# Performance work log

Measured on AMD Instinct MI355X. Metric: run time of the kernel, lower is better.

The kernel has to match this reference:

```python
import jax, jax.numpy as jnp
import numpy as np

DIM = 2048
HEAD_DIM = 128
H = DIM // HEAD_DIM          # num ttt heads = 16
D_H = 128                    # inter_multi = 1.0 -> d_h = head_dim
CHUNK = 2048                 # lact_chunk_size
B, L = 1, 8192
BASE_LR = 0.01
LN_EPS = 1e-6                # flax LayerNorm default
NS_COEFS = [(4.0848, -6.8946, 2.927), (3.9505, -6.3029, 2.6377),
            (3.7418, -5.5913, 2.3037), (2.8769, -3.1427, 1.2046),
            (2.8366, -3.0525, 1.2012)]


def silu(x):
    return x * jax.nn.sigmoid(x)


def silu_backprop(dy, x):
    s = jax.nn.sigmoid(x)
    return dy * s * (1 + x * (1 - s))


def l2_norm(x, eps=1e-5):
    return x / (jnp.linalg.norm(x, axis=-1, keepdims=True) + eps)


def zeropower_ns5(G):
    # 5-step Newton-Schulz orthogonalization on a batch of matrices (bh, m, n)
    X = G
    transposed = G.shape[1] > G.shape[2]
    if transposed:
        X = jnp.swapaxes(X, 1, 2)
    X = X / (jnp.linalg.norm(X, axis=(1, 2), keepdims=True) + 1e-7)
    for a, b, c in NS_COEFS:
        A = X @ jnp.swapaxes(X, 1, 2)
        Bm = b * A + c * (A @ A)
        X = a * X + Bm @ X
    if transposed:
        X = jnp.swapaxes(X, 1, 2)
    return X


def block_causal_lact_swiglu(w0, w1, w2, q, k, v, lr0, lr1, lr2, momentum):
    # w0,w2: (bh, d_h, d); w1: (bh, d, d_h); q,k,v: (bh, l, d); lr*: (bh, l, 1)
    bh, l, d = k.shape
    v = jnp.swapaxes(v, 1, 2)   # (bh, d, l)
    q = jnp.swapaxes(q, 1, 2)   # (bh, d, l)
    w0_norm = jnp.linalg.norm(w0, axis=2, keepdims=True)
    w1_norm = jnp.linalg.norm(w1, axis=2, keepdims=True)
    w2_norm = jnp.linalg.norm(w2, axis=2, keepdims=True)
    outs = []
    for i in range(0, l - CHUNK, CHUNK):
        s, e = i, i + CHUNK
        ki = k[:, s:e, :]                      # (bh, C, d)
        vi = v[:, :, s:e]                      # (bh, d, C)
        qi = q[:, :, s:e]                      # (bh, d, C)
        lr0i, lr1i, lr2i = lr0[:, s:e, :], lr1[:, s:e, :], lr2[:, s:e, :]
        # apply current fast weights to queries
        h = w2 @ qi                            # (bh, d_h, C)
        gate = silu(w0 @ qi)
        outs.append(w1 @ (gate * h))           # (bh, d, C)
        # manual SwiGLU backprop through keys to get fast-weight grads
        kiT = jnp.swapaxes(ki, 1, 2)           # (bh, d, C)
        gate_before = w0 @ kiT                 # (bh, d_h, C)
        hidden_before = w2 @ kiT               # (bh, d_h, C)
        hidden = silu(gate_before) * hidden_before
        dhidden = jnp.swapaxes(w1, 1, 2) @ vi  # (bh, d_h, C)
        dhidden_before = dhidden * silu(gate_before)
        dgate = dhidden * hidden_before
        dgate_before = silu_backprop(dgate, gate_before)
        lr1iT = jnp.swapaxes(lr1i, 1, 2)       # (bh, 1, C) per-token lr
        dw1 = vi @ jnp.swapaxes(hidden * lr1iT, 1, 2)   # (bh, d, d_h)
        dw0 = dgate_before @ (ki * lr0i)                # (bh, d_h, d)
        dw2 = dhidden_before @ (ki * lr2i)              # (bh, d_h, d)
        if momentum is not None:
            m_i = jnp.mean(momentum[:, s:e, :], axis=1, keepdims=True)  # (bh,1,1)
            dw0 = dw0 + dw0 * m_i
            dw1 = dw1 + dw1 * m_i
            dw2 = dw2 + dw2 * m_i
        dw0 = zeropower_ns5(dw0)
        dw1 = zeropower_ns5(dw1)
        dw2 = zeropower_ns5(dw2)
        w0 = w0 + dw0
        w1 = w1 + dw1
        w2 = w2 + dw2
        # renormalize rows back to the initial norms
        w0 = w0 / (jnp.linalg.norm(w0, axis=2, keepdims=True) + 1e-5) * w0_norm
        w1 = w1 / (jnp.linalg.norm(w1, axis=2, keepdims=True) + 1e-5) * w1_norm
        w2 = w2 / (jnp.linalg.norm(w2, axis=2, keepdims=True) + 1e-5) * w2_norm
    # final chunk: apply only
    qi = q[:, :, l - CHUNK:]
    h = w2 @ qi
    gate = silu(w0 @ qi)
    outs.append(w1 @ (gate * h))
    out = jnp.concatenate(outs, axis=2)        # (bh, d, l)
    return jnp.swapaxes(out, 1, 2)             # (bh, l, d)


def _forward(x, W_qkv, W_lr, W_o, W_m, b_m, W_s, b_s, ln_g, ln_b, w0, w1, w2):
    b, l, _ = x.shape
    h, d = H, HEAD_DIM
    qkv = silu(x @ W_qkv).reshape(b, l, h, 3 * d)
    ttt_q, ttt_k, ttt_v = jnp.split(qkv, 3, axis=-1)
    ttt_q = l2_norm(ttt_q).reshape(b * h, l, d)
    ttt_k = l2_norm(ttt_k).reshape(b * h, l, d)
    ttt_v = ttt_v.reshape(b * h, l, d)
    base_lr_inv = BASE_LR + jnp.log(-jnp.expm1(jnp.float32(-BASE_LR)))
    lr = jax.nn.softplus(x @ W_lr + base_lr_inv)                 # (b, l, 3h)
    lr = lr.reshape(b, l, 3, h).transpose(2, 0, 3, 1).reshape(3, b * h, l, 1)
    lr0, lr1, lr2 = lr[0], lr[1], lr[2]
    w0b = jnp.tile(w0, (b, 1, 1))
    w1b = jnp.tile(w1, (b, 1, 1))
    w2b = jnp.tile(w2, (b, 1, 1))
    momentum = jax.nn.sigmoid(x @ W_m + b_m)                     # (b, l, h)
    momentum = momentum.reshape(b, l, h, 1).transpose(0, 2, 1, 3).reshape(b * h, l, 1)
    out = block_causal_lact_swiglu(w0b, w1b, w2b, ttt_q, ttt_k, ttt_v,
                                   lr0, lr1, lr2, momentum)      # (bh, l, d)
    # LayerNorm over last dim (flax default eps)
    mu = jnp.mean(out, axis=-1, keepdims=True)
    var = jnp.mean(jnp.square(out - mu), axis=-1, keepdims=True)
    out = (out - mu) * jax.lax.rsqrt(var + LN_EPS) * ln_g + ln_b
    scale = silu(x @ W_s + b_s).reshape(b, l, h, 1).transpose(0, 2, 1, 3).reshape(b * h, l, 1)
    out = out * scale
    out = out.reshape(b, h, l, d).transpose(0, 2, 1, 3).reshape(b, l, h * d)
    return out @ W_o


def setup_inputs() -> dict:
    ks = jax.random.split(jax.random.key(0), 11)
    sd = 1.0 / np.sqrt(DIM)
    return {
        "x": jax.random.normal(ks[0], (B, L, DIM), jnp.float32),
        "W_qkv": jax.random.normal(ks[1], (DIM, 3 * DIM), jnp.float32) * sd,
        "W_lr": jax.random.normal(ks[2], (DIM, 3 * H), jnp.float32) * sd,
        "W_o": jax.random.normal(ks[3], (DIM, DIM), jnp.float32) * sd,
        "W_m": jax.random.normal(ks[4], (DIM, H), jnp.float32) * sd,
        "b_m": jnp.zeros((H,), jnp.float32),
        "W_s": jax.random.normal(ks[5], (DIM, H), jnp.float32) * sd,
        "b_s": jnp.zeros((H,), jnp.float32),
        "ln_g": jnp.ones((HEAD_DIM,), jnp.float32),
        "ln_b": jnp.zeros((HEAD_DIM,), jnp.float32),
        "w0": jax.random.normal(ks[6], (H, D_H, HEAD_DIM), jnp.float32) / np.sqrt(HEAD_DIM),
        "w1": jax.random.normal(ks[7], (H, HEAD_DIM, D_H), jnp.float32) / np.sqrt(D_H),
        "w2": jax.random.normal(ks[8], (H, D_H, HEAD_DIM), jnp.float32) / np.sqrt(HEAD_DIM),
    }


def reference(x, W_qkv, W_lr, W_o, W_m, b_m, W_s, b_s, ln_g, ln_b, w0, w1, w2):
    return _forward(x, W_qkv, W_lr, W_o, W_m, b_m, W_s, b_s, ln_g, ln_b, w0, w1, w2)
```

## Files before the change

### kernel.cpp

```cpp
#include <hip/hip_runtime.h>
#include <hip/hip_bf16.h>
#include <cstdint>
#include <cstddef>

#define LSEQ   8192
#define DMODEL 2048
#define NH     16
#define HD     128
#define CH     2048

typedef __attribute__((ext_vector_type(8))) __bf16 bf16x8;
typedef __attribute__((ext_vector_type(4))) float f32x4;


__device__ __forceinline__ float wave_sum64(float v) {
#pragma unroll
  for (int m = 32; m; m >>= 1) v += __shfl_xor(v, m, 64);
  return v;
}

__device__ __forceinline__ float sigm(float x) { return 1.0f / (1.0f + expf(-x)); }

__device__ __forceinline__ unsigned short f2bf(float f) {
  unsigned int u = __float_as_uint(f);
  u += 0x7FFFu + ((u >> 16) & 1u);
  return (unsigned short)(u >> 16);
}
__device__ __forceinline__ float bf2f(unsigned short h) {
  return __uint_as_float((unsigned int)h << 16);
}

__device__ __forceinline__ void gload_lds16(const void* g, void* l) {
  __builtin_amdgcn_global_load_lds((__attribute__((address_space(1))) void*)(g),
                                   (__attribute__((address_space(3))) void*)(l), 16, 0, 0);
}

union bfu8 { bf16x8 v; unsigned short u[8]; };


__global__ void k_cast(const float* __restrict__ X, unsigned short* __restrict__ Xb, int n4) {
  int i = blockIdx.x * 256 + threadIdx.x;
  int stride = gridDim.x * 256;
  for (; i < n4; i += stride) {
    float4 v = ((const float4*)X)[i];
    ushort4 o;
    o.x = f2bf(v.x); o.y = f2bf(v.y); o.z = f2bf(v.z); o.w = f2bf(v.w);
    ((ushort4*)Xb)[i] = o;
  }
}

__global__ void k_tcast(const float* __restrict__ W, unsigned short* __restrict__ Wt,
                        int K, int N) {
  __shared__ float t[64][65];
  const int n0 = blockIdx.x * 64, k0 = blockIdx.y * 64;
  const int tid = threadIdx.x;
  const int cx = tid & 63, ry = tid >> 6;
#pragma unroll
  for (int r = 0; r < 16; ++r) {
    int row = ry + r * 4;
    t[row][cx] = W[(size_t)(k0 + row) * N + n0 + cx];
  }
  __syncthreads();
#pragma unroll
  for (int r = 0; r < 16; ++r) {
    int nn = ry + r * 4;
    Wt[(size_t)(n0 + nn) * K + k0 + cx] = f2bf(t[cx][nn]);
  }
}


__device__ __forceinline__ void gemm_core(const unsigned short* __restrict__ A,
                                          const unsigned short* __restrict__ B,
                                          int K, int ldA, int ldB, int row0, int col0,
                                          unsigned short* Al, unsigned short* Bl,
                                          f32x4 acc[4][4]) {
  const int tid = threadIdx.x;
  const int w = tid >> 6, l = tid & 63;
  const int lrow = l & 15, lk = (l >> 4) * 8;
  const int wr = (w >> 1) * 64, wc = (w & 1) * 64;
  const int srow = l >> 2, skk = (l & 3) * 8;

  for (int kk = 0; kk < K; kk += 32) {
#pragma unroll
    for (int q = 0; q < 2; ++q) {
      int c = w * 2 + q;
      gload_lds16(A + (size_t)(row0 + c * 16 + srow) * ldA + kk + skk, &Al[c * 512]);
      gload_lds16(B + (size_t)(col0 + c * 16 + srow) * ldB + kk + skk, &Bl[c * 512]);
    }
    __syncthreads();
    bf16x8 af[4], bfr[4];
#pragma unroll
    for (int m = 0; m < 4; ++m)
      af[m] = *(const bf16x8*)&Al[(wr + m * 16 + lrow) * 32 + lk];
#pragma unroll
    for (int n = 0; n < 4; ++n)
      bfr[n] = *(const bf16x8*)&Bl[(wc + n * 16 + lrow) * 32 + lk];
#pragma unroll
    for (int m = 0; m < 4; ++m)
#pragma unroll
      for (int n = 0; n < 4; ++n)
        acc[m][n] = __builtin_amdgcn_mfma_f32_16x16x32_bf16(af[m], bfr[n], acc[m][n], 0, 0, 0);
    __syncthreads();
  }
}


__device__ __forceinline__ bf16x8 ld_sw(const unsigned short* base, int row, int kcol) {
  int byte = (row * 256 + kcol * 2) ^ ((row & 7) << 4);
  return *(const bf16x8*)((const char*)base + byte);
}
__device__ __forceinline__ void st_sw(unsigned short* base, int row, int col, unsigned short v) {
  int byte = (row * 256 + col * 2) ^ ((row & 7) << 4);
  *(unsigned short*)((char*)base + byte) = v;
}
__device__ __forceinline__ unsigned short ld_sw1(const unsigned short* base, int row, int col) {
  int byte = (row * 256 + col * 2) ^ ((row & 7) << 4);
  return *(const unsigned short*)((const char*)base + byte);
}

__device__ __forceinline__ void stage_sw(const float* __restrict__ src, int ld,
                                         unsigned short* dst, int tid) {
#pragma unroll
  for (int p = 0; p < 16; ++p) {
    int row = p * 8 + (tid >> 5);
    int col = (tid & 31) * 4;
    float4 v = *(const float4*)(src + (size_t)row * ld + col);
    int byte = (row * 256 + col * 2) ^ ((row & 7) << 4);
    unsigned short* d = (unsigned short*)((char*)dst + byte);
    d[0] = f2bf(v.x); d[1] = f2bf(v.y); d[2] = f2bf(v.z); d[3] = f2bf(v.w);
  }
}

__device__ __forceinline__ void stage_sw64(const float* __restrict__ src, int ld,
                                           unsigned short* dst, int tid) {
#pragma unroll
  for (int p = 0; p < 8; ++p) {
    int row = p * 8 + (tid >> 5);
    int col = (tid & 31) * 4;
    float4 v = *(const float4*)(src + (size_t)row * ld + col);
    int byte = (row * 256 + col * 2) ^ ((row & 7) << 4);
    unsigned short* d = (unsigned short*)((char*)dst + byte);
    d[0] = f2bf(v.x); d[1] = f2bf(v.y); d[2] = f2bf(v.z); d[3] = f2bf(v.w);
  }
}

__device__ __forceinline__ void stage_hl(const float* __restrict__ src, int ld,
                                         unsigned short* H, unsigned short* L, int tid) {
#pragma unroll
  for (int p = 0; p < 16; ++p) {
    int row = p * 8 + (tid >> 5);
    int col = (tid & 31) * 4;
    float4 v = *(const float4*)(src + (size_t)row * ld + col);
    int byte = (row * 256 + col * 2) ^ ((row & 7) << 4);
    unsigned short* h = (unsigned short*)((char*)H + byte);
    unsigned short* l = (unsigned short*)((char*)L + byte);
    const float* pv = (const float*)&v;
#pragma unroll
    for (int i = 0; i < 4; ++i) {
      unsigned short hi = f2bf(pv[i]);
      h[i] = hi;
      l[i] = f2bf(pv[i] - bf2f(hi));
    }
  }
}

__device__ __forceinline__ void stage_hl_1024(const float* __restrict__ src, int ld,
                                              unsigned short* H, unsigned short* L, int tid) {
#pragma unroll
  for (int p = 0; p < 4; ++p) {
    int row = p * 32 + (tid >> 5);
    int col = (tid & 31) * 4;
    float4 v = *(const float4*)(src + (size_t)row * ld + col);
    int byte = (row * 256 + col * 2) ^ ((row & 7) << 4);
    unsigned short* h = (unsigned short*)((char*)H + byte);
    unsigned short* l = (unsigned short*)((char*)L + byte);
    const float* pv = (const float*)&v;
#pragma unroll
    for (int i = 0; i < 4; ++i) {
      unsigned short hi = f2bf(pv[i]);
      h[i] = hi;
      l[i] = f2bf(pv[i] - bf2f(hi));
    }
  }
}

__device__ __forceinline__ void stage_hl_ts(const float* __restrict__ src, int ld,
                                            const float* __restrict__ lr,
                                            unsigned short* H, unsigned short* L, int tid) {
#pragma unroll
  for (int p = 0; p < 16; ++p) {
    int t = p * 8 + (tid >> 5);
    int d = (tid & 31) * 4;
    float4 v = *(const float4*)(src + (size_t)t * ld + d);
    float sc = lr[t];
    const float* pv = (const float*)&v;
#pragma unroll
    for (int i = 0; i < 4; ++i) {
      float x = pv[i] * sc;
      unsigned short hi = f2bf(x);
      st_sw(H, d + i, t, hi);
      st_sw(L, d + i, t, f2bf(x - bf2f(hi)));
    }
  }
}


__global__ void k_init_w(const float* __restrict__ w0, const float* __restrict__ w1,
                         const float* __restrict__ w2, float* __restrict__ WW,
                         float* __restrict__ WN0, float* __restrict__ W1T) {
  int rid = blockIdx.x;
  int m = rid >> 11;
  int gr = rid & 2047;
  const float* src = (m == 0) ? w0 : (m == 1) ? w1 : w2;
  const float* row = src + (size_t)gr * HD;
  float* drow = WW + ((size_t)m * 2048 + gr) * HD;
  int l = threadIdx.x;
  float v0 = row[l], v1 = row[l + 64];
  drow[l] = v0; drow[l + 64] = v1;
  if (m == 1) {
    int g = gr >> 7, r = gr & 127;
    W1T[((size_t)g * 128 + l) * 128 + r] = v0;
    W1T[((size_t)g * 128 + l + 64) * 128 + r] = v1;
  }
  float s = wave_sum64(v0 * v0 + v1 * v1);
  if (l == 0) WN0[rid] = sqrtf(s);
}


__global__ __launch_bounds__(256) void k_qkv_mfma(const unsigned short* __restrict__ xb,
                                                  const unsigned short* __restrict__ Wqt,
                                                  float* __restrict__ Q, float* __restrict__ Km,
                                                  float* __restrict__ V) {
  __shared__ unsigned short Al[128 * 32];
  __shared__ unsigned short Bl[128 * 32];
  __shared__ float nrm[128][2];
  const int bx = blockIdx.x, ct = blockIdx.y;

  f32x4 acc[4][4];
#pragma unroll
  for (int m = 0; m < 4; ++m)
#pragma unroll
    for (int n = 0; n < 4; ++n) acc[m][n] = {};

  gemm_core(xb, Wqt, DMODEL, DMODEL, DMODEL, bx * 128, ct * 128, Al, Bl, acc);

  const int hh = ct / 3, which = ct % 3;
  float* dst = (which == 0) ? Q : (which == 1) ? Km : V;
  const int tid = threadIdx.x, w = tid >> 6, l = tid & 63;
  const int wr = (w >> 1) * 64, wc = (w & 1) * 64;

#pragma unroll
  for (int m = 0; m < 4; ++m)
#pragma unroll
    for (int n = 0; n < 4; ++n)
#pragma unroll
      for (int j = 0; j < 4; ++j) {
        float v = acc[m][n][j];
        acc[m][n][j] = v * sigm(v);
      }

  float f[4][4];
  if (which != 2) {
#pragma unroll
    for (int m = 0; m < 4; ++m)
#pragma unroll
      for (int j = 0; j < 4; ++j) {
        float p = 0.0f;
#pragma unroll
        for (int n = 0; n < 4; ++n) p = fmaf(acc[m][n][j], acc[m][n][j], p);
        p += __shfl_xor(p, 1, 64);
        p += __shfl_xor(p, 2, 64);
        p += __shfl_xor(p, 4, 64);
        p += __shfl_xor(p, 8, 64);
        f[m][j] = p;
      }
    if ((l & 15) == 0) {
#pragma unroll
      for (int m = 0; m < 4; ++m)
#pragma unroll
        for (int j = 0; j < 4; ++j)
          nrm[wr + m * 16 + (l >> 4) * 4 + j][w & 1] = f[m][j];
    }
    __syncthreads();
#pragma unroll
    for (int m = 0; m < 4; ++m)
#pragma unroll
      for (int j = 0; j < 4; ++j) {
        int row = wr + m * 16 + (l >> 4) * 4 + j;
        f[m][j] = 1.0f / (sqrtf(nrm[row][0] + nrm[row][1]) + 1e-5f);
      }
  } else {
#pragma unroll
    for (int m = 0; m < 4; ++m)
#pragma unroll
      for (int j = 0; j < 4; ++j) f[m][j] = 1.0f;
  }

#pragma unroll
  for (int m = 0; m < 4; ++m)
#pragma unroll
    for (int j = 0; j < 4; ++j) {
      int t = bx * 128 + wr + m * 16 + (l >> 4) * 4 + j;
      int fth = t * NH + hh;
      int g = fth >> 13, tp = fth & 8191;
      float* drow = dst + ((size_t)g * LSEQ + tp) * HD;
#pragma unroll
      for (int n = 0; n < 4; ++n)
        drow[wc + n * 16 + (l & 15)] = acc[m][n][j] * f[m][j];
    }
}


__global__ __launch_bounds__(256) void k_lrms5(const float* __restrict__ x,
                                               const float* __restrict__ Wlr,
                                               const float* __restrict__ Wsc,
                                               float* __restrict__ P) {
  __shared__ float Xs[128][67];
  __shared__ float Ws[128][68];
  const int tb = blockIdx.x;
  const int kp = blockIdx.y;
  const int tid = threadIdx.x;
  for (int i = tid; i < 128 * 64; i += 256) {
    int k = i >> 6, c = i & 63;
    float wv = (c < 48) ? Wlr[(size_t)(kp * 128 + k) * 48 + c]
                        : Wsc[(size_t)(kp * 128 + k) * 16 + (c - 48)];
    Ws[k][c] = wv;
  }
  const int t8 = tid >> 5, kk = tid & 31;
#pragma unroll
  for (int r = 0; r < 8; ++r) {
    int t = t8 + r * 8;
    float4 v = *(const float4*)(x + (size_t)(tb * 64 + t) * DMODEL + kp * 128 + kk * 4);
    Xs[kk * 4 + 0][t] = v.x; Xs[kk * 4 + 1][t] = v.y;
    Xs[kk * 4 + 2][t] = v.z; Xs[kk * 4 + 3][t] = v.w;
  }
  __syncthreads();
  const int ty = tid >> 4, tx = tid & 15;
  float acc[4][4];
#pragma unroll
  for (int i = 0; i < 4; ++i)
#pragma unroll
    for (int j = 0; j < 4; ++j) acc[i][j] = 0.0f;
  for (int k = 0; k < 128; ++k) {
    float a[4], b[4];
#pragma unroll
    for (int i = 0; i < 4; ++i) a[i] = Xs[k][ty * 4 + i];
#pragma unroll
    for (int j = 0; j < 4; ++j) b[j] = Ws[k][tx * 4 + j];
#pragma unroll
    for (int i = 0; i < 4; ++i)
#pragma unroll
      for (int j = 0; j < 4; ++j) acc[i][j] = fmaf(a[i], b[j], acc[i][j]);
  }
  float* o = P + ((size_t)tb * 16 + kp) * 4096;
#pragma unroll
  for (int i = 0; i < 4; ++i)
#pragma unroll
    for (int j = 0; j < 4; ++j)
      o[(ty * 4 + i) * 64 + tx * 4 + j] = acc[i][j];
}

__global__ void k_lrsum(const float* __restrict__ P, const float* __restrict__ bs,
                        float* __restrict__ LR, float* __restrict__ SCL) {
  int e = blockIdx.x * 256 + threadIdx.x;
  int t = e >> 6, c = e & 63;
  const float* base = P + ((size_t)(t >> 6) * 16) * 4096 + (t & 63) * 64 + c;
  float sum = 0.0f;
#pragma unroll
  for (int kp = 0; kp < 16; ++kp) sum += base[(size_t)kp * 4096];
  if (c < 48) {
    float base_lr_inv = 0.01f + logf(-expm1f(-0.01f));
    float v = sum + base_lr_inv;
    float sp = fmaxf(v, 0.0f) + log1pf(expf(-fabsf(v)));
    LR[(size_t)c * LSEQ + t] = sp;
  } else {
    float v = sum + bs[c - 48];
    SCL[(size_t)(c - 48) * LSEQ + t] = v * sigm(v);
  }
}


__global__ __launch_bounds__(256) void k_out2(const float* __restrict__ WW,
                                              const float* __restrict__ Q,
                                              const float* __restrict__ SCL,
                                              const float* __restrict__ lng,
                                              const float* __restrict__ lnb,
                                              unsigned short* __restrict__ U, int s) {
  __shared__ __align__(16) char smem[81920];
  unsigned short* Qs  = (unsigned short*)smem;
  unsigned short* W0s = (unsigned short*)(smem + 16384);
  unsigned short* W2s = (unsigned short*)(smem + 49152);
  float* Os = (float*)(smem + 16384);

  const int g = blockIdx.y;
  const int t0 = blockIdx.x * 64;
  const int tid = threadIdx.x;
  const int w = tid >> 6, l = tid & 63;
  const int lrow = l & 15, lk8 = (l >> 4) * 8;
  const int wr = (w >> 1) * 32, wc = (w & 1) * 64;

  const float* Qg  = Q + ((size_t)g * LSEQ + s + t0) * HD;
  const float* w0g = WW + ((size_t)0 * 2048 + g * 128) * 128;
  const float* w1g = WW + ((size_t)1 * 2048 + g * 128) * 128;
  const float* w2g = WW + ((size_t)2 * 2048 + g * 128) * 128;

  stage_sw64(Qg, HD, Qs, tid);
  stage_sw(w0g, 128, W0s, tid);
  stage_sw(w2g, 128, W2s, tid);
  __syncthreads();

  f32x4 ga[2][4], ha[2][4];
#pragma unroll
  for (int m = 0; m < 2; ++m)
#pragma unroll
    for (int n = 0; n < 4; ++n) { ga[m][n] = {}; ha[m][n] = {}; }
#pragma unroll
  for (int kk = 0; kk < 128; kk += 32) {
    bf16x8 af[2], b0[4], b2[4];
#pragma unroll
    for (int m = 0; m < 2; ++m) af[m] = ld_sw(Qs, wr + m * 16 + lrow, kk + lk8);
#pragma unroll
    for (int n = 0; n < 4; ++n) {
      b0[n] = ld_sw(W0s, wc + n * 16 + lrow, kk + lk8);
      b2[n] = ld_sw(W2s, wc + n * 16 + lrow, kk + lk8);
    }
#pragma unroll
    for (int m = 0; m < 2; ++m)
#pragma unroll
      for (int n = 0; n < 4; ++n) {
        ga[m][n] = __builtin_amdgcn_mfma_f32_16x16x32_bf16(af[m], b0[n], ga[m][n], 0, 0, 0);
        ha[m][n] = __builtin_amdgcn_mfma_f32_16x16x32_bf16(af[m], b2[n], ha[m][n], 0, 0, 0);
      }
  }
  __syncthreads();
#pragma unroll
  for (int m = 0; m < 2; ++m)
#pragma unroll
    for (int n = 0; n < 4; ++n)
#pragma unroll
      for (int j = 0; j < 4; ++j) {
        int row = wr + m * 16 + (l >> 4) * 4 + j;
        int col = wc + n * 16 + (l & 15);
        float gv = ga[m][n][j];
        st_sw(Qs, row, col, f2bf(gv * sigm(gv) * ha[m][n][j]));
      }
  stage_sw(w1g, 128, W0s, tid);
  __syncthreads();

  f32x4 oa[2][4];
#pragma unroll
  for (int m = 0; m < 2; ++m)
#pragma unroll
    for (int n = 0; n < 4; ++n) oa[m][n] = {};
#pragma unroll
  for (int kk = 0; kk < 128; kk += 32) {
    bf16x8 af[2], b1[4];
#pragma unroll
    for (int m = 0; m < 2; ++m) af[m] = ld_sw(Qs, wr + m * 16 + lrow, kk + lk8);
#pragma unroll
    for (int n = 0; n < 4; ++n) b1[n] = ld_sw(W0s, wc + n * 16 + lrow, kk + lk8);
#pragma unroll
    for (int m = 0; m < 2; ++m)
#pragma unroll
      for (int n = 0; n < 4; ++n)
        oa[m][n] = __builtin_amdgcn_mfma_f32_16x16x32_bf16(af[m], b1[n], oa[m][n], 0, 0, 0);
  }
  __syncthreads();
#pragma unroll
  for (int m = 0; m < 2; ++m)
#pragma unroll
    for (int n = 0; n < 4; ++n)
#pragma unroll
      for (int j = 0; j < 4; ++j) {
        int row = wr + m * 16 + (l >> 4) * 4 + j;
        int col = wc + n * 16 + (l & 15);
        Os[row * 132 + col] = oa[m][n][j];
      }
  __syncthreads();

  const int tok = tid >> 2, part = tid & 3;
  const float* orow = Os + tok * 132 + part * 32;
  float sum = 0.0f;
#pragma unroll
  for (int q = 0; q < 8; ++q) {
    float4 v = *(const float4*)(orow + q * 4);
    sum += (v.x + v.y) + (v.z + v.w);
  }
  sum += __shfl_xor(sum, 1, 64);
  sum += __shfl_xor(sum, 2, 64);
  float mu = sum * (1.0f / 128.0f);
  float vs = 0.0f;
#pragma unroll
  for (int q = 0; q < 8; ++q) {
    float4 v = *(const float4*)(orow + q * 4);
    float d0 = v.x - mu, d1 = v.y - mu, d2 = v.z - mu, d3 = v.w - mu;
    vs += d0 * d0 + d1 * d1 + d2 * d2 + d3 * d3;
  }
  vs += __shfl_xor(vs, 1, 64);
  vs += __shfl_xor(vs, 2, 64);
  float rstd = rsqrtf(vs * (1.0f / 128.0f) + 1e-6f);
  int tabs = s + t0 + tok;
  float sc = SCL[(size_t)g * LSEQ + tabs];
  unsigned short* urow = U + (size_t)tabs * DMODEL + g * HD + part * 32;
#pragma unroll
  for (int q = 0; q < 8; ++q) {
    float4 v = *(const float4*)(orow + q * 4);
    int d = part * 32 + q * 4;
    ushort4 o;
    o.x = f2bf(((v.x - mu) * rstd * lng[d + 0] + lnb[d + 0]) * sc);
    o.y = f2bf(((v.y - mu) * rstd * lng[d + 1] + lnb[d + 1]) * sc);
    o.z = f2bf(((v.z - mu) * rstd * lng[d + 2] + lnb[d + 2]) * sc);
    o.w = f2bf(((v.w - mu) * rstd * lng[d + 3] + lnb[d + 3]) * sc);
    *(ushort4*)(urow + q * 4) = o;
  }
}


__global__ __launch_bounds__(1024) void k_fe(const float* __restrict__ WW,
                                             const float* __restrict__ W1T,
                                             const float* __restrict__ Km,
                                             const float* __restrict__ V,
                                             float* __restrict__ BUF, int s) {
  __shared__ __align__(16) char smem[131072];
  unsigned short* KH = (unsigned short*)smem;
  unsigned short* KL = (unsigned short*)(smem + 32768);
  unsigned short* VH = (unsigned short*)(smem + 65536);
  unsigned short* VL = (unsigned short*)(smem + 98304);

  const int tt0 = blockIdx.x * 128;
  const int g = blockIdx.y;
  const int tid = threadIdx.x;
  const int w = tid >> 6, l = tid & 63;
  const int ww = w >> 2, wv = w & 3;
  const int lrow = l & 15, lk8 = (l >> 4) * 8;
  const int frow = (l >> 4) * 4, fcol = l & 15;

  stage_hl_1024(Km + ((size_t)g * LSEQ + s + tt0) * HD, HD, KH, KL, tid);
  stage_hl_1024(V + ((size_t)g * LSEQ + s + tt0) * HD, HD, VH, VL, tid);
  __syncthreads();

  const float* Asrc[3];
  Asrc[0] = WW + ((size_t)0 * 2048 + g * 128) * 128;
  Asrc[1] = WW + ((size_t)2 * 2048 + g * 128) * 128;
  Asrc[2] = W1T + (size_t)g * 16384;

  f32x4 acc[3][2][2];
#pragma unroll
  for (int q = 0; q < 3; ++q)
#pragma unroll
    for (int m = 0; m < 2; ++m)
#pragma unroll
      for (int n = 0; n < 2; ++n) acc[q][m][n] = {};

#pragma unroll 1
  for (int q = 0; q < 3; ++q) {
    const float* src = Asrc[q];
    const unsigned short* BH = (q == 2) ? VH : KH;
    const unsigned short* BL = (q == 2) ? VL : KL;
#pragma unroll
    for (int kk = 0; kk < 128; kk += 32) {
      bf16x8 ah[2], al[2], bh[2], bl[2];
#pragma unroll
      for (int m = 0; m < 2; ++m) {
        int row = ww * 32 + m * 16 + lrow;
        float4 v0 = *(const float4*)(src + (size_t)row * 128 + kk + lk8);
        float4 v1 = *(const float4*)(src + (size_t)row * 128 + kk + lk8 + 4);
        bfu8 h, lo;
        const float* p0 = (const float*)&v0;
        const float* p1 = (const float*)&v1;
#pragma unroll
        for (int i = 0; i < 4; ++i) {
          unsigned short hb0 = f2bf(p0[i]);
          h.u[i] = hb0; lo.u[i] = f2bf(p0[i] - bf2f(hb0));
          unsigned short hb1 = f2bf(p1[i]);
          h.u[i + 4] = hb1; lo.u[i + 4] = f2bf(p1[i] - bf2f(hb1));
        }
        ah[m] = h.v; al[m] = lo.v;
      }
#pragma unroll
      for (int n = 0; n < 2; ++n) {
        int row = wv * 32 + n * 16 + lrow;
        bh[n] = ld_sw(BH, row, kk + lk8);
        bl[n] = ld_sw(BL, row, kk + lk8);
      }
#pragma unroll
      for (int m = 0; m < 2; ++m)
#pragma unroll
        for (int n = 0; n < 2; ++n) {
          acc[q][m][n] = __builtin_amdgcn_mfma_f32_16x16x32_bf16(ah[m], bh[n], acc[q][m][n], 0, 0, 0);
          acc[q][m][n] = __builtin_amdgcn_mfma_f32_16x16x32_bf16(ah[m], bl[n], acc[q][m][n], 0, 0, 0);
          acc[q][m][n] = __builtin_amdgcn_mfma_f32_16x16x32_bf16(al[m], bh[n], acc[q][m][n], 0, 0, 0);
        }
    }
  }

  float* out0 = BUF + (size_t)0 * (NH * 128 * CH) + (size_t)g * 128 * CH;
  float* out1 = BUF + (size_t)1 * (NH * 128 * CH) + (size_t)g * 128 * CH;
  float* out2 = BUF + (size_t)2 * (NH * 128 * CH) + (size_t)g * 128 * CH;
#pragma unroll
  for (int m = 0; m < 2; ++m)
#pragma unroll
    for (int n = 0; n < 2; ++n)
#pragma unroll
      for (int j = 0; j < 4; ++j) {
        int row = ww * 32 + m * 16 + frow + j;
        int col = wv * 32 + n * 16 + fcol;
        float gb = acc[0][m][n][j];
        float hb = acc[1][m][n][j];
        float dh = acc[2][m][n][j];
        float sg = sigm(gb);
        float sgb = gb * sg;
        float hid = sgb * hb;
        float dgate = dh * hb;
        float dgb = dgate * sg * (1.0f + gb * (1.0f - sg));
        float dhb = dh * sgb;
        size_t o = (size_t)row * CH + tt0 + col;
        out0[o] = hid; out1[o] = dgb; out2[o] = dhb;
      }
}

__global__ __launch_bounds__(256) void k_dwp_mx(const float* __restrict__ BUF,
                                                const float* __restrict__ Km,
                                                const float* __restrict__ V,
                                                const float* __restrict__ LR,
                                                float* __restrict__ DWP, int s) {
  __shared__ __align__(16) char smem[131072];
  unsigned short* AH = (unsigned short*)smem;
  unsigned short* AL = (unsigned short*)(smem + 32768);
  unsigned short* BH = (unsigned short*)(smem + 65536);
  unsigned short* BL = (unsigned short*)(smem + 98304);

  const int p = blockIdx.x;
  const int g = blockIdx.y;
  const int z = blockIdx.z;
  const int tid = threadIdx.x;
  const int w = tid >> 6, l = tid & 63;
  const int lrow = l & 15, lk8 = (l >> 4) * 8;
  const int wr = (w >> 1) * 64, wc = (w & 1) * 64;

  const int msel = (z == 0) ? 1 : (z == 1) ? 0 : 2;
  const float* M = BUF + (size_t)msel * (NH * 128 * CH) + (size_t)g * 128 * CH;
  const float* N = (z == 1) ? V : Km;
  const float* lr = LR + (size_t)(z * NH + g) * LSEQ;
  const int ts = p * 256;

  f32x4 acc[4][4];
#pragma unroll
  for (int m = 0; m < 4; ++m)
#pragma unroll
    for (int n = 0; n < 4; ++n) acc[m][n] = {};

  for (int h = 0; h < 2; ++h) {
    if (h) __syncthreads();
    stage_hl(M + ts + h * 128, CH, AH, AL, tid);
    stage_hl_ts(N + ((size_t)g * LSEQ + s + ts + h * 128) * HD, HD,
                lr + s + ts + h * 128, BH, BL, tid);
    __syncthreads();
#pragma unroll
    for (int kk = 0; kk < 128; kk += 32) {
      bf16x8 ah[4], al4[4], bh[4], bl4[4];
#pragma unroll
      for (int m = 0; m < 4; ++m) {
        ah[m] = ld_sw(AH, wr + m * 16 + lrow, kk + lk8);
        al4[m] = ld_sw(AL, wr + m * 16 + lrow, kk + lk8);
      }
#pragma unroll
      for (int n = 0; n < 4; ++n) {
        bh[n] = ld_sw(BH, wc + n * 16 + lrow, kk + lk8);
        bl4[n] = ld_sw(BL, wc + n * 16 + lrow, kk + lk8);
      }
#pragma unroll
      for (int m = 0; m < 4; ++m)
#pragma unroll
        for (int n = 0; n < 4; ++n) {
          acc[m][n] = __builtin_amdgcn_mfma_f32_16x16x32_bf16(ah[m], bh[n], acc[m][n], 0, 0, 0);
          acc[m][n] = __builtin_amdgcn_mfma_f32_16x16x32_bf16(ah[m], bl4[n], acc[m][n], 0, 0, 0);
          acc[m][n] = __builtin_amdgcn_mfma_f32_16x16x32_bf16(al4[m], bh[n], acc[m][n], 0, 0, 0);
        }
    }
  }

  float* outp = DWP + (((size_t)(z * NH + g)) * 8 + p) * 16384;
#pragma unroll
  for (int m = 0; m < 4; ++m)
#pragma unroll
    for (int n = 0; n < 4; ++n)
#pragma unroll
      for (int j = 0; j < 4; ++j) {
        int row = wr + m * 16 + (l >> 4) * 4 + j;
        int col = wc + n * 16 + (l & 15);
        outp[row * 128 + col] = acc[m][n][j];
      }
}

__global__ __launch_bounds__(1024) void k_ns5_mfma(const float* __restrict__ DWP,
                                                   float* __restrict__ DW) {
  __shared__ __align__(16) char smem[131072];
  unsigned short* PH = (unsigned short*)smem;
  unsigned short* PL = (unsigned short*)(smem + 32768);
  unsigned short* QH = (unsigned short*)(smem + 65536);
  unsigned short* QL = (unsigned short*)(smem + 98304);
  float* red = (float*)(smem + 65536);

  const float NA[5] = {4.0848f, 3.9505f, 3.7418f, 2.8769f, 2.8366f};
  const float NB[5] = {-6.8946f, -6.3029f, -5.5913f, -3.1427f, -3.0525f};
  const float NC[5] = {2.927f, 2.6377f, 2.3037f, 1.2046f, 1.2012f};
  const int zg = blockIdx.x;
  const int z = zg >> 4;
  const float* base = DWP + (size_t)zg * 8 * 16384;
  float* Gout = DW + (size_t)zg * 16384;
  const int tid = threadIdx.x;
  const int w = tid >> 6, l = tid & 63;
  const int ww = w >> 2, wv = w & 3;
  const int lrow = l & 15, lk8 = (l >> 4) * 8;
  const int frow = (l >> 4) * 4, fcol = l & 15;

  float vals[16];
  float psum = 0.0f;
#pragma unroll
  for (int r = 0; r < 16; ++r) {
    int idx = tid + r * 1024;
    float sv = 0.0f;
#pragma unroll
    for (int p = 0; p < 8; ++p) sv += base[(size_t)p * 16384 + idx];
    vals[r] = sv;
    psum = fmaf(sv, sv, psum);
  }
  psum = wave_sum64(psum);
  if (l == 0) red[w] = psum;
  __syncthreads();
  float tot = 0.0f;
#pragma unroll
  for (int i = 0; i < 16; ++i) tot += red[i];
  float scl = 1.0f / (sqrtf(tot) + 1e-7f);
  __syncthreads();
#pragma unroll
  for (int r = 0; r < 16; ++r) {
    int idx = tid + r * 1024;
    int rr = idx >> 7, cc = idx & 127;
    float v = vals[r] * scl;
    unsigned short hi = f2bf(v);
    st_sw(PH, rr, cc, hi);
    st_sw(PL, rr, cc, f2bf(v - bf2f(hi)));
  }
  __syncthreads();

#pragma unroll 1
  for (int it = 0; it < 5; ++it) {
    const float ac = NA[it], bc = NB[it], cc2 = NC[it];

    f32x4 accA[2][2];
#pragma unroll
    for (int m = 0; m < 2; ++m)
#pragma unroll
      for (int n = 0; n < 2; ++n) accA[m][n] = {};
#pragma unroll
    for (int kk = 0; kk < 128; kk += 32) {
      bf16x8 ah[2], al[2], bh[2], bl[2];
#pragma unroll
      for (int m = 0; m < 2; ++m) {
        ah[m] = ld_sw(PH, ww * 32 + m * 16 + lrow, kk + lk8);
        al[m] = ld_sw(PL, ww * 32 + m * 16 + lrow, kk + lk8);
      }
#pragma unroll
      for (int n = 0; n < 2; ++n) {
        bh[n] = ld_sw(PH, wv * 32 + n * 16 + lrow, kk + lk8);
        bl[n] = ld_sw(PL, wv * 32 + n * 16 + lrow, kk + lk8);
      }
#pragma unroll
      for (int m = 0; m < 2; ++m)
#pragma unroll
        for (int n = 0; n < 2; ++n) {
          accA[m][n] = __builtin_amdgcn_mfma_f32_16x16x32_bf16(ah[m], bh[n], accA[m][n], 0, 0, 0);
          accA[m][n] = __builtin_amdgcn_mfma_f32_16x16x32_bf16(ah[m], bl[n], accA[m][n], 0, 0, 0);
          accA[m][n] = __builtin_amdgcn_mfma_f32_16x16x32_bf16(al[m], bh[n], accA[m][n], 0, 0, 0);
        }
    }
#pragma unroll
    for (int m = 0; m < 2; ++m)
#pragma unroll
      for (int n = 0; n < 2; ++n)
#pragma unroll
        for (int j = 0; j < 4; ++j) {
          int row = ww * 32 + m * 16 + frow + j;
          int col = wv * 32 + n * 16 + fcol;
          float v = accA[m][n][j];
          unsigned short hi = f2bf(v);
          st_sw(QH, row, col, hi);
          st_sw(QL, row, col, f2bf(v - bf2f(hi)));
        }
    __syncthreads();

    f32x4 accB[2][2];
#pragma unroll
    for (int m = 0; m < 2; ++m)
#pragma unroll
      for (int n = 0; n < 2; ++n) accB[m][n] = {};
#pragma unroll
    for (int kk = 0; kk < 128; kk += 32) {
      bf16x8 ah[2], al[2], bh[2], bl[2];
#pragma unroll
      for (int m = 0; m < 2; ++m) {
        ah[m] = ld_sw(QH, ww * 32 + m * 16 + lrow, kk + lk8);
        al[m] = ld_sw(QL, ww * 32 + m * 16 + lrow, kk + lk8);
      }
#pragma unroll
      for (int n = 0; n < 2; ++n) {
        bh[n] = ld_sw(QH, wv * 32 + n * 16 + lrow, kk + lk8);
        bl[n] = ld_sw(QL, wv * 32 + n * 16 + lrow, kk + lk8);
      }
#pragma unroll
      for (int m = 0; m < 2; ++m)
#pragma unroll
        for (int n = 0; n < 2; ++n) {
          accB[m][n] = __builtin_amdgcn_mfma_f32_16x16x32_bf16(ah[m], bh[n], accB[m][n], 0, 0, 0);
          accB[m][n] = __builtin_amdgcn_mfma_f32_16x16x32_bf16(ah[m], bl[n], accB[m][n], 0, 0, 0);
          accB[m][n] = __builtin_amdgcn_mfma_f32_16x16x32_bf16(al[m], bh[n], accB[m][n], 0, 0, 0);
        }
    }
#pragma unroll
    for (int m = 0; m < 2; ++m)
#pragma unroll
      for (int n = 0; n < 2; ++n)
#pragma unroll
        for (int j = 0; j < 4; ++j)
          accB[m][n][j] = fmaf(bc, accA[m][n][j], cc2 * accB[m][n][j]);
    __syncthreads();
#pragma unroll
    for (int m = 0; m < 2; ++m)
#pragma unroll
      for (int n = 0; n < 2; ++n)
#pragma unroll
        for (int j = 0; j < 4; ++j) {
          int row = ww * 32 + m * 16 + frow + j;
          int col = wv * 32 + n * 16 + fcol;
          float v = accB[m][n][j];
          unsigned short hi = f2bf(v);
          st_sw(QH, row, col, hi);
          st_sw(QL, row, col, f2bf(v - bf2f(hi)));
        }
    unsigned short th[16], tl[16];
#pragma unroll
    for (int r = 0; r < 16; ++r) {
      int idx = tid + r * 1024;
      int rr = idx >> 7, ccx = idx & 127;
      th[r] = ld_sw1(PH, rr, ccx);
      tl[r] = ld_sw1(PL, rr, ccx);
    }
    __syncthreads();
#pragma unroll
    for (int r = 0; r < 16; ++r) {
      int idx = tid + r * 1024;
      int rr = idx >> 7, ccx = idx & 127;
      st_sw(PH, ccx, rr, th[r]);
      st_sw(PL, ccx, rr, tl[r]);
    }
    __syncthreads();

    f32x4 accC[2][2];
#pragma unroll
    for (int m = 0; m < 2; ++m)
#pragma unroll
      for (int n = 0; n < 2; ++n) accC[m][n] = {};
#pragma unroll
    for (int kk = 0; kk < 128; kk += 32) {
      bf16x8 ah[2], al[2], bh[2], bl[2];
#pragma unroll
      for (int m = 0; m < 2; ++m) {
        ah[m] = ld_sw(PH, ww * 32 + m * 16 + lrow, kk + lk8);
        al[m] = ld_sw(PL, ww * 32 + m * 16 + lrow, kk + lk8);
      }
#pragma unroll
      for (int n = 0; n < 2; ++n) {
        bh[n] = ld_sw(QH, wv * 32 + n * 16 + lrow, kk + lk8);
        bl[n] = ld_sw(QL, wv * 32 + n * 16 + lrow, kk + lk8);
      }
#pragma unroll
      for (int m = 0; m < 2; ++m)
#pragma unroll
        for (int n = 0; n < 2; ++n) {
          accC[m][n] = __builtin_amdgcn_mfma_f32_16x16x32_bf16(ah[m], bh[n], accC[m][n], 0, 0, 0);
          accC[m][n] = __builtin_amdgcn_mfma_f32_16x16x32_bf16(ah[m], bl[n], accC[m][n], 0, 0, 0);
          accC[m][n] = __builtin_amdgcn_mfma_f32_16x16x32_bf16(al[m], bh[n], accC[m][n], 0, 0, 0);
        }
    }
#pragma unroll
    for (int m = 0; m < 2; ++m)
#pragma unroll
      for (int n = 0; n < 2; ++n)
#pragma unroll
        for (int j = 0; j < 4; ++j) {
          int row = ww * 32 + m * 16 + frow + j;
          int col = wv * 32 + n * 16 + fcol;
          float yv = bf2f(ld_sw1(PH, row, col)) + bf2f(ld_sw1(PL, row, col));
          accC[m][n][j] = fmaf(ac, yv, accC[m][n][j]);
        }
    __syncthreads();
#pragma unroll
    for (int m = 0; m < 2; ++m)
#pragma unroll
      for (int n = 0; n < 2; ++n)
#pragma unroll
        for (int j = 0; j < 4; ++j) {
          int row = ww * 32 + m * 16 + frow + j;
          int col = wv * 32 + n * 16 + fcol;
          float v = accC[m][n][j];
          unsigned short hi = f2bf(v);
          st_sw(PH, row, col, hi);
          st_sw(PL, row, col, f2bf(v - bf2f(hi)));
        }
    __syncthreads();
  }

#pragma unroll
  for (int r = 0; r < 16; ++r) {
    int idx = tid + r * 1024;
    int rr = idx >> 7, ccx = idx & 127;
    if (z == 1)
      Gout[idx] = bf2f(ld_sw1(PH, rr, ccx)) + bf2f(ld_sw1(PL, rr, ccx));
    else
      Gout[idx] = bf2f(ld_sw1(PH, ccx, rr)) + bf2f(ld_sw1(PL, ccx, rr));
  }
}

__global__ void k_apply(float* __restrict__ WW, const float* __restrict__ DW,
                        const float* __restrict__ WN0, float* __restrict__ W1T) {
  int rid = blockIdx.x;
  int m = rid >> 11;
  int gr = rid & 2047;
  int l = threadIdx.x;
  float* wrow = WW + (size_t)rid * 128;
  const float* drow = DW + (size_t)rid * 128;
  float v0 = wrow[l] + drow[l];
  float v1 = wrow[l + 64] + drow[l + 64];
  float s = wave_sum64(v0 * v0 + v1 * v1);
  float f = WN0[rid] / (sqrtf(s) + 1e-5f);
  v0 *= f; v1 *= f;
  wrow[l] = v0;
  wrow[l + 64] = v1;
  if (m == 1) {
    int g = gr >> 7, r = gr & 127;
    W1T[((size_t)g * 128 + l) * 128 + r] = v0;
    W1T[((size_t)g * 128 + l + 64) * 128 + r] = v1;
  }
}


__global__ __launch_bounds__(256) void k_final_mfma(const unsigned short* __restrict__ U,
                                                    const unsigned short* __restrict__ Wot,
                                                    float* __restrict__ out) {
  __shared__ unsigned short Al[128 * 32];
  __shared__ unsigned short Bl[128 * 32];
  f32x4 acc[4][4];
#pragma unroll
  for (int m = 0; m < 4; ++m)
#pragma unroll
    for (int n = 0; n < 4; ++n) acc[m][n] = {};

  const int row0 = blockIdx.x * 128, col0 = blockIdx.y * 128;
  gemm_core(U, Wot, DMODEL, DMODEL, DMODEL, row0, col0, Al, Bl, acc);

  const int tid = threadIdx.x, w = tid >> 6, l = tid & 63;
  const int wr = (w >> 1) * 64, wc = (w & 1) * 64;
#pragma unroll
  for (int m = 0; m < 4; ++m)
#pragma unroll
    for (int j = 0; j < 4; ++j) {
      int t = row0 + wr + m * 16 + (l >> 4) * 4 + j;
      float* orow = out + (size_t)t * DMODEL + col0;
#pragma unroll
      for (int n = 0; n < 4; ++n)
        orow[wc + n * 16 + (l & 15)] = acc[m][n][j];
    }
}


extern "C" void kernel_launch(void* const* d_in, const int* in_sizes, int n_in,
                              void* d_out, int out_size, void* d_ws, size_t ws_size,
                              hipStream_t stream) {
  (void)in_sizes; (void)n_in; (void)out_size;
  const float* x    = (const float*)d_in[0];
  const float* Wqkv = (const float*)d_in[1];
  const float* Wlr  = (const float*)d_in[2];
  const float* Wo   = (const float*)d_in[3];
  const float* Wsc  = (const float*)d_in[6];
  const float* bs   = (const float*)d_in[7];
  const float* lng  = (const float*)d_in[8];
  const float* lnb  = (const float*)d_in[9];
  const float* w0   = (const float*)d_in[10];
  const float* w1   = (const float*)d_in[11];
  const float* w2   = (const float*)d_in[12];

  float* Q = (float*)d_out;

  float* ws = (float*)d_ws;
  size_t off = 0;
  auto alloc = [&](size_t n) { float* p = ws + off; off += n; return p; };
  float* Km   = alloc((size_t)NH * LSEQ * HD);
  float* V    = alloc((size_t)NH * LSEQ * HD);
  float* Uf   = alloc((size_t)LSEQ * DMODEL / 2);
  float* LR   = alloc((size_t)3 * NH * LSEQ);
  float* SCL  = alloc((size_t)NH * LSEQ);
  float* WW   = alloc((size_t)3 * NH * HD * HD);
  float* WN0  = alloc((size_t)3 * NH * HD);
  float* W1T  = alloc((size_t)NH * HD * HD);
  float* BUF  = alloc((size_t)3 * NH * HD * CH);
  float* DW   = alloc((size_t)3 * NH * HD * HD);
  float* DWP  = alloc((size_t)3 * NH * 8 * HD * HD);
  if (off * sizeof(float) > ws_size) return;

  unsigned short* U = (unsigned short*)Uf;
  unsigned short* xb  = (unsigned short*)BUF;
  unsigned short* Wqt = (unsigned short*)(BUF + (size_t)LSEQ * DMODEL / 2);
  float* Plr = BUF;
  unsigned short* Wot = (unsigned short*)BUF;

  k_init_w<<<3 * NH * HD, 64, 0, stream>>>(w0, w1, w2, WW, WN0, W1T);
  k_cast<<<2048, 256, 0, stream>>>(x, xb, LSEQ * DMODEL / 4);
  k_tcast<<<dim3(3 * DMODEL / 64, DMODEL / 64), 256, 0, stream>>>(Wqkv, Wqt, DMODEL, 3 * DMODEL);
  k_qkv_mfma<<<dim3(LSEQ / 128, 48), 256, 0, stream>>>(xb, Wqt, Q, Km, V);
  k_lrms5<<<dim3(LSEQ / 64, 16), 256, 0, stream>>>(x, Wlr, Wsc, Plr);
  k_lrsum<<<LSEQ * 64 / 256, 256, 0, stream>>>(Plr, bs, LR, SCL);

  for (int c = 0; c < 4; ++c) {
    int s = c * CH;
    k_out2<<<dim3(CH / 64, NH), 256, 0, stream>>>(WW, Q, SCL, lng, lnb, U, s);
    if (c < 3) {
      k_fe<<<dim3(CH / 128, NH), 1024, 0, stream>>>(WW, W1T, Km, V, BUF, s);
      k_dwp_mx<<<dim3(8, NH, 3), 256, 0, stream>>>(BUF, Km, V, LR, DWP, s);
      k_ns5_mfma<<<3 * NH, 1024, 0, stream>>>(DWP, DW);
      k_apply<<<3 * NH * HD, 64, 0, stream>>>(WW, DW, WN0, W1T);
    }
  }
  k_tcast<<<dim3(DMODEL / 64, DMODEL / 64), 256, 0, stream>>>(Wo, Wot, DMODEL, DMODEL);
  k_final_mfma<<<dim3(LSEQ / 128, DMODEL / 128), 256, 0, stream>>>(U, Wot, (float*)d_out);
}
```

Measured before the change: 1.347 ms.

## Rewrite QKV projection GEMM with 256x256 tiles and 4-stage LDS pipeline

Replaces the 128x128-tile QKV GEMM with a 512-thread kernel that computes 256x256 tiles. It uses direct global-to-LDS loads into a 4-slot swizzled shared-memory ring, prefetches two stages ahead, and uses setprio around the MFMA blocks. The fused SiLU, L2-norm and scatter epilogue is adapted to the new wave layout. The goal is more data reuse per tile and less memory stall in the largest GEMM. In exchange it uses 128KB of LDS per block, so occupancy is lower and there are fewer blocks to fill the GPU.

```diff
diff --git a/kernel.cpp b/kernel.cpp
--- a/kernel.cpp
+++ b/kernel.cpp
@@ -227,86 +227,159 @@
 }
 
 
-__global__ __launch_bounds__(256) void k_qkv_mfma(const unsigned short* __restrict__ xb,
-                                                  const unsigned short* __restrict__ Wqt,
-                                                  float* __restrict__ Q, float* __restrict__ Km,
-                                                  float* __restrict__ V) {
-  __shared__ unsigned short Al[128 * 32];
-  __shared__ unsigned short Bl[128 * 32];
-  __shared__ float nrm[128][2];
-  const int bx = blockIdx.x, ct = blockIdx.y;
-
-  f32x4 acc[4][4];
-#pragma unroll
-  for (int m = 0; m < 4; ++m)
+__device__ __forceinline__ bf16x8 ldf8(const char* slotm, int row, int kc) {
+  int f = (((row & 3) ^ ((row >> 2) & 3)) << 4);
+  int byte = (row * 64 + kc * 2) ^ f;
+  return *(const bf16x8*)(slotm + byte);
+}
+
+__global__ __launch_bounds__(512, 2) void k_qkv8(const unsigned short* __restrict__ A,
+                                                 const unsigned short* __restrict__ B,
+                                                 float* __restrict__ Q, float* __restrict__ Km,
+                                                 float* __restrict__ V) {
+  __shared__ __align__(16) char smem[131072];
+  const int tid = threadIdx.x;
+  const int w = tid >> 6, l = tid & 63;
+  const int wm = w >> 2, wn = w & 3;
+  const int lrow = l & 15, lk8 = (l >> 4) * 8;
+  const int row0 = blockIdx.x * 256, col0 = blockIdx.y * 256;
+  const int NK = DMODEL / 32;
+
+  const int r0 = tid >> 2;
+  const int ks0 = ((tid & 3) * 8) ^ ((((r0 & 3) ^ ((r0 >> 2) & 3))) << 3);
+
+  const unsigned short* gA = A + (size_t)(row0 + r0) * DMODEL + ks0;
+  const unsigned short* gB = B + (size_t)(col0 + r0) * DMODEL + ks0;
+
+#define SLOT(s)   (smem + (s) * 32768)
+#define STAGE_A8(s, j) { const unsigned short* g = gA + (j) * 32;                 \
+    gload_lds16(g, SLOT(s) + w * 1024);                                           \
+    gload_lds16(g + (size_t)128 * DMODEL, SLOT(s) + 8192 + w * 1024); }
+#define STAGE_B8(s, j) { const unsigned short* g = gB + (j) * 32;                 \
+    gload_lds16(g, SLOT(s) + 16384 + w * 1024);                                   \
+    gload_lds16(g + (size_t)128 * DMODEL, SLOT(s) + 16384 + 8192 + w * 1024); }
+
+  f32x4 acc[8][4];
+#pragma unroll
+  for (int m = 0; m < 8; ++m)
 #pragma unroll
     for (int n = 0; n < 4; ++n) acc[m][n] = {};
 
-  gemm_core(xb, Wqt, DMODEL, DMODEL, DMODEL, bx * 128, ct * 128, Al, Bl, acc);
-
+  STAGE_A8(0, 0); STAGE_B8(0, 0);
+  STAGE_A8(1, 1); STAGE_B8(1, 1);
+  asm volatile("s_waitcnt vmcnt(4)");
+  __builtin_amdgcn_s_barrier();
+  __builtin_amdgcn_sched_barrier(0);
+
+#pragma unroll 1
+  for (int j = 0; j < NK; ++j) {
+    const int s = j & 3;
+    const char* As = SLOT(s);
+    const char* Bs = SLOT(s) + 16384;
+    bf16x8 af[8];
+#pragma unroll
+    for (int m = 0; m < 8; ++m) af[m] = ldf8(As, wm * 128 + m * 16 + lrow, lk8);
+    bf16x8 b0 = ldf8(Bs, wn * 64 + 0 * 16 + lrow, lk8);
+    bf16x8 b1 = ldf8(Bs, wn * 64 + 1 * 16 + lrow, lk8);
+    if (j + 2 < NK) STAGE_A8((j + 2) & 3, j + 2);
+    __builtin_amdgcn_s_barrier();
+    __builtin_amdgcn_s_setprio(1);
+#pragma unroll
+    for (int m = 0; m < 8; ++m) {
+      acc[m][0] = __builtin_amdgcn_mfma_f32_16x16x32_bf16(af[m], b0, acc[m][0], 0, 0, 0);
+      acc[m][1] = __builtin_amdgcn_mfma_f32_16x16x32_bf16(af[m], b1, acc[m][1], 0, 0, 0);
+    }
+    __builtin_amdgcn_s_setprio(0);
+    __builtin_amdgcn_s_barrier();
+    bf16x8 b2 = ldf8(Bs, wn * 64 + 2 * 16 + lrow, lk8);
+    bf16x8 b3 = ldf8(Bs, wn * 64 + 3 * 16 + lrow, lk8);
+    if (j + 2 < NK) STAGE_B8((j + 2) & 3, j + 2);
+    __builtin_amdgcn_s_barrier();
+    __builtin_amdgcn_s_setprio(1);
+#pragma unroll
+    for (int m = 0; m < 8; ++m) {
+      acc[m][2] = __builtin_amdgcn_mfma_f32_16x16x32_bf16(af[m], b2, acc[m][2], 0, 0, 0);
+      acc[m][3] = __builtin_amdgcn_mfma_f32_16x16x32_bf16(af[m], b3, acc[m][3], 0, 0, 0);
+    }
+    __builtin_amdgcn_s_setprio(0);
+    if (j + 2 < NK) asm volatile("s_waitcnt vmcnt(4)");
+    else            asm volatile("s_waitcnt vmcnt(0)");
+    __builtin_amdgcn_s_barrier();
+    __builtin_amdgcn_sched_barrier(0);
+  }
+#undef SLOT
+#undef STAGE_A8
+#undef STAGE_B8
+
+  const int ct = blockIdx.y * 2 + (wn >> 1);
   const int hh = ct / 3, which = ct % 3;
   float* dst = (which == 0) ? Q : (which == 1) ? Km : V;
-  const int tid = threadIdx.x, w = tid >> 6, l = tid & 63;
-  const int wr = (w >> 1) * 64, wc = (w & 1) * 64;
-
-#pragma unroll
-  for (int m = 0; m < 4; ++m)
+  float* nrm = (float*)smem;
+
+#pragma unroll
+  for (int m = 0; m < 8; ++m)
 #pragma unroll
     for (int n = 0; n < 4; ++n)
 #pragma unroll
-      for (int j = 0; j < 4; ++j) {
-        float v = acc[m][n][j];
-        acc[m][n][j] = v * sigm(v);
-      }
-
-  float f[4][4];
+      for (int jj = 0; jj < 4; ++jj) {
+        float v = acc[m][n][jj];
+        acc[m][n][jj] = v * sigm(v);
+      }
+
+  float f[8][4];
+#pragma unroll
+  for (int m = 0; m < 8; ++m)
+#pragma unroll
+    for (int jj = 0; jj < 4; ++jj) f[m][jj] = 1.0f;
+
   if (which != 2) {
 #pragma unroll
-    for (int m = 0; m < 4; ++m)
-#pragma unroll
-      for (int j = 0; j < 4; ++j) {
+    for (int m = 0; m < 8; ++m)
+#pragma unroll
+      for (int jj = 0; jj < 4; ++jj) {
         float p = 0.0f;
 #pragma unroll
-        for (int n = 0; n < 4; ++n) p = fmaf(acc[m][n][j], acc[m][n][j], p);
+        for (int n = 0; n < 4; ++n) p = fmaf(acc[m][n][jj], acc[m][n][jj], p);
         p += __shfl_xor(p, 1, 64);
         p += __shfl_xor(p, 2, 64);
         p += __shfl_xor(p, 4, 64);
         p += __shfl_xor(p, 8, 64);
-        f[m][j] = p;
+        f[m][jj] = p;
       }
     if ((l & 15) == 0) {
 #pragma unroll
-      for (int m = 0; m < 4; ++m)
-#pragma unroll
-        for (int j = 0; j < 4; ++j)
-          nrm[wr + m * 16 + (l >> 4) * 4 + j][w & 1] = f[m][j];
-    }
-    __syncthreads();
-#pragma unroll
-    for (int m = 0; m < 4; ++m)
-#pragma unroll
-      for (int j = 0; j < 4; ++j) {
-        int row = wr + m * 16 + (l >> 4) * 4 + j;
-        f[m][j] = 1.0f / (sqrtf(nrm[row][0] + nrm[row][1]) + 1e-5f);
-      }
-  } else {
-#pragma unroll
-    for (int m = 0; m < 4; ++m)
-#pragma unroll
-      for (int j = 0; j < 4; ++j) f[m][j] = 1.0f;
-  }
-
-#pragma unroll
-  for (int m = 0; m < 4; ++m)
-#pragma unroll
-    for (int j = 0; j < 4; ++j) {
-      int t = bx * 128 + wr + m * 16 + (l >> 4) * 4 + j;
+      for (int m = 0; m < 8; ++m)
+#pragma unroll
+        for (int jj = 0; jj < 4; ++jj) {
+          int row = wm * 128 + m * 16 + (l >> 4) * 4 + jj;
+          nrm[row * 4 + (wn >> 1) * 2 + (wn & 1)] = f[m][jj];
+        }
+    }
+  }
+  __syncthreads();
+  if (which != 2) {
+#pragma unroll
+    for (int m = 0; m < 8; ++m)
+#pragma unroll
+      for (int jj = 0; jj < 4; ++jj) {
+        int row = wm * 128 + m * 16 + (l >> 4) * 4 + jj;
+        float s2 = nrm[row * 4 + (wn >> 1) * 2 + 0] + nrm[row * 4 + (wn >> 1) * 2 + 1];
+        f[m][jj] = 1.0f / (sqrtf(s2) + 1e-5f);
+      }
+  }
+
+#pragma unroll
+  for (int m = 0; m < 8; ++m)
+#pragma unroll
+    for (int jj = 0; jj < 4; ++jj) {
+      int row = wm * 128 + m * 16 + (l >> 4) * 4 + jj;
+      int t = row0 + row;
       int fth = t * NH + hh;
       int g = fth >> 13, tp = fth & 8191;
-      float* drow = dst + ((size_t)g * LSEQ + tp) * HD;
+      float* drow = dst + ((size_t)g * LSEQ + tp) * HD + (wn & 1) * 64;
 #pragma unroll
       for (int n = 0; n < 4; ++n)
-        drow[wc + n * 16 + (l & 15)] = acc[m][n][j] * f[m][j];
+        drow[n * 16 + (l & 15)] = acc[m][n][jj] * f[m][jj];
     }
 }
 
@@ -1018,7 +1091,7 @@
   k_init_w<<<3 * NH * HD, 64, 0, stream>>>(w0, w1, w2, WW, WN0, W1T);
   k_cast<<<2048, 256, 0, stream>>>(x, xb, LSEQ * DMODEL / 4);
   k_tcast<<<dim3(3 * DMODEL / 64, DMODEL / 64), 256, 0, stream>>>(Wqkv, Wqt, DMODEL, 3 * DMODEL);
-  k_qkv_mfma<<<dim3(LSEQ / 128, 48), 256, 0, stream>>>(xb, Wqt, Q, Km, V);
+  k_qkv8<<<dim3(LSEQ / 256, 3 * DMODEL / 256), 512, 0, stream>>>(xb, Wqt, Q, Km, V);
   k_lrms5<<<dim3(LSEQ / 64, 16), 256, 0, stream>>>(x, Wlr, Wsc, Plr);
   k_lrsum<<<LSEQ * 64 / 256, 256, 0, stream>>>(Plr, bs, LR, SCL);
 
```

After: 1.343 ms. Within noise of the previous version (-0.3%).
